# Performance work log

Hardware: AMD Instinct MI355X
Metric: run time of the kernel (lower is better)

## Reference

```python
import jax, jax.numpy as jnp
import numpy as np

N_NODES = 50000
N_EDGES = 800000
D_FEAT = 64


def setup_inputs() -> dict:
    key = jax.random.key(0)
    k1, k2, k3, k4 = jax.random.split(key, 4)
    row_idx = jnp.sort(jax.random.randint(k1, (N_EDGES,), 0, N_NODES, dtype=jnp.int32))
    col_idx = jax.random.randint(k2, (N_EDGES,), 0, N_NODES, dtype=jnp.int32)
    vals = jax.random.uniform(k3, (N_EDGES,), dtype=jnp.float32)
    embeds = jax.random.normal(k4, (N_NODES, D_FEAT), dtype=jnp.float32)
    return {"row_idx": row_idx, "col_idx": col_idx, "vals": vals, "embeds": embeds}


def reference(row_idx, col_idx, vals, embeds):
    # SpMM: out[r] = sum_{e: row[e]==r} vals[e] * embeds[col[e]]
    gathered = vals[:, None] * embeds[col_idx]          # [E, D]
    out = jax.ops.segment_sum(gathered, row_idx, num_segments=N_NODES)  # [N, D]
    return out
```

## Files before the change

kernel.cpp:

```cpp
#include <hip/hip_runtime.h>


constexpr int N_NODES = 50000;
constexpr int N_EDGES = 800000;
constexpr int D_FEAT  = 64;

__global__ __launch_bounds__(256) void build_row_ptr_kernel(
    const int* __restrict__ row_idx,
    int*       __restrict__ row_ptr)
{
    const int e = blockIdx.x * blockDim.x + threadIdx.x;
    if (e >= N_EDGES) return;
    const int r     = row_idx[e];
    const int rprev = (e == 0) ? -1 : row_idx[e - 1];
    for (int q = rprev + 1; q <= r; ++q) row_ptr[q] = e;
    if (e == N_EDGES - 1) {
        for (int q = r + 1; q <= N_NODES; ++q) row_ptr[q] = N_EDGES;
    }
}

__global__ __launch_bounds__(256) void gcn_spmm_rows_kernel(
    const int*   __restrict__ row_ptr,
    const int*   __restrict__ col_idx,
    const float* __restrict__ vals,
    const float* __restrict__ embeds,
    float*       __restrict__ out)
{
    const int gtid = blockIdx.x * blockDim.x + threadIdx.x;
    const int row  = gtid >> 6;
    const int lane = threadIdx.x & 63;
    if (row >= N_NODES) return;

    const int s = row_ptr[row];
    const int e = row_ptr[row + 1];

    float a0 = 0.f, a1 = 0.f, a2 = 0.f, a3 = 0.f;

    for (int base = s; base < e; base += 64) {
        const int n = (e - base < 64) ? (e - base) : 64;

        int   c = 0;
        float v = 0.f;
        if (lane < n) {
            c = col_idx[base + lane];
            v = vals[base + lane];
        }

        int j = 0;
        for (; j + 4 <= n; j += 4) {
            const int   c0 = __shfl(c, j);
            const int   c1 = __shfl(c, j + 1);
            const int   c2 = __shfl(c, j + 2);
            const int   c3 = __shfl(c, j + 3);
            const float v0 = __shfl(v, j);
            const float v1 = __shfl(v, j + 1);
            const float v2 = __shfl(v, j + 2);
            const float v3 = __shfl(v, j + 3);
            const float g0 = embeds[c0 * D_FEAT + lane];
            const float g1 = embeds[c1 * D_FEAT + lane];
            const float g2 = embeds[c2 * D_FEAT + lane];
            const float g3 = embeds[c3 * D_FEAT + lane];
            a0 += v0 * g0;
            a1 += v1 * g1;
            a2 += v2 * g2;
            a3 += v3 * g3;
        }
        for (; j < n; ++j) {
            const int   cj = __shfl(c, j);
            const float vj = __shfl(v, j);
            a0 += vj * embeds[cj * D_FEAT + lane];
        }
    }

    out[row * D_FEAT + lane] = (a0 + a1) + (a2 + a3);
}

extern "C" void kernel_launch(void* const* d_in, const int* in_sizes, int n_in,
                              void* d_out, int out_size, void* d_ws, size_t ws_size,
                              hipStream_t stream) {
    const int*   row_idx = (const int*)  d_in[0];
    const int*   col_idx = (const int*)  d_in[1];
    const float* vals    = (const float*)d_in[2];
    const float* embeds  = (const float*)d_in[3];
    float*       out     = (float*)      d_out;
    int*         row_ptr = (int*)        d_ws;

    {
        const int block  = 256;
        const int blocks = (N_EDGES + block - 1) / block;
        build_row_ptr_kernel<<<blocks, block, 0, stream>>>(row_idx, row_ptr);
    }

    {
        const int block  = 256;
        const int blocks = (N_NODES * 64 + block - 1) / block;
        gcn_spmm_rows_kernel<<<blocks, block, 0, stream>>>(row_ptr, col_idx, vals,
                                                           embeds, out);
    }
}
```

Before: 103.5 us.

## Split each row's edges across four sub-groups with float4 gathers and shuffle reduction

Each 64-lane wavefront now handles a row as four 16-lane groups. Each group reads a different edge directly and gathers the full 64-float embedding row as float4 loads, instead of broadcasting indices through shuffles and loading one float per lane. The partial sums are combined with xor shuffles, and one group writes a float4 result. This cuts the shuffle overhead and raises memory-level parallelism per row, in exchange for a reduction at the end and somewhat less coalesced loads of the edge indices.

```diff
diff --git a/kernel.cpp b/kernel.cpp
--- a/kernel.cpp
+++ b/kernel.cpp
@@ -28,51 +28,50 @@
 {
     const int gtid = blockIdx.x * blockDim.x + threadIdx.x;
     const int row  = gtid >> 6;
+    if (row >= N_NODES) return;
     const int lane = threadIdx.x & 63;
-    if (row >= N_NODES) return;
+    const int q    = lane >> 4;
+    const int f    = lane & 15;
 
     const int s = row_ptr[row];
     const int e = row_ptr[row + 1];
 
-    float a0 = 0.f, a1 = 0.f, a2 = 0.f, a3 = 0.f;
+    const float4* __restrict__ emb4 = (const float4*)embeds;
 
-    for (int base = s; base < e; base += 64) {
-        const int n = (e - base < 64) ? (e - base) : 64;
+    float4 a0 = make_float4(0.f, 0.f, 0.f, 0.f);
+    float4 a1 = make_float4(0.f, 0.f, 0.f, 0.f);
 
-        int   c = 0;
-        float v = 0.f;
-        if (lane < n) {
-            c = col_idx[base + lane];
-            v = vals[base + lane];
-        }
-
-        int j = 0;
-        for (; j + 4 <= n; j += 4) {
-            const int   c0 = __shfl(c, j);
-            const int   c1 = __shfl(c, j + 1);
-            const int   c2 = __shfl(c, j + 2);
-            const int   c3 = __shfl(c, j + 3);
-            const float v0 = __shfl(v, j);
-            const float v1 = __shfl(v, j + 1);
-            const float v2 = __shfl(v, j + 2);
-            const float v3 = __shfl(v, j + 3);
-            const float g0 = embeds[c0 * D_FEAT + lane];
-            const float g1 = embeds[c1 * D_FEAT + lane];
-            const float g2 = embeds[c2 * D_FEAT + lane];
-            const float g3 = embeds[c3 * D_FEAT + lane];
-            a0 += v0 * g0;
-            a1 += v1 * g1;
-            a2 += v2 * g2;
-            a3 += v3 * g3;
-        }
-        for (; j < n; ++j) {
-            const int   cj = __shfl(c, j);
-            const float vj = __shfl(v, j);
-            a0 += vj * embeds[cj * D_FEAT + lane];
-        }
+    int base = s + q;
+    for (; base + 4 < e; base += 8) {
+        const int   c0 = col_idx[base];
+        const float v0 = vals[base];
+        const int   c1 = col_idx[base + 4];
+        const float v1 = vals[base + 4];
+        const float4 g0 = emb4[c0 * 16 + f];
+        const float4 g1 = emb4[c1 * 16 + f];
+        a0.x += v0 * g0.x; a0.y += v0 * g0.y; a0.z += v0 * g0.z; a0.w += v0 * g0.w;
+        a1.x += v1 * g1.x; a1.y += v1 * g1.y; a1.z += v1 * g1.z; a1.w += v1 * g1.w;
+    }
+    if (base < e) {
+        const int   c0 = col_idx[base];
+        const float v0 = vals[base];
+        const float4 g0 = emb4[c0 * 16 + f];
+        a0.x += v0 * g0.x; a0.y += v0 * g0.y; a0.z += v0 * g0.z; a0.w += v0 * g0.w;
     }
 
-    out[row * D_FEAT + lane] = (a0 + a1) + (a2 + a3);
+    float x = a0.x + a1.x;
+    float y = a0.y + a1.y;
+    float z = a0.z + a1.z;
+    float w = a0.w + a1.w;
+
+    x += __shfl_xor(x, 16); x += __shfl_xor(x, 32);
+    y += __shfl_xor(y, 16); y += __shfl_xor(y, 32);
+    z += __shfl_xor(z, 16); z += __shfl_xor(z, 32);
+    w += __shfl_xor(w, 16); w += __shfl_xor(w, 32);
+
+    if (q == 0) {
+        ((float4*)out)[row * 16 + f] = make_float4(x, y, z, w);
+    }
 }
 
 extern "C" void kernel_launch(void* const* d_in, const int* in_sizes, int n_in,
@@ -90,7 +89,6 @@
         const int blocks = (N_EDGES + block - 1) / block;
         build_row_ptr_kernel<<<blocks, block, 0, stream>>>(row_idx, row_ptr);
     }
-
     {
         const int block  = 256;
         const int blocks = (N_NODES * 64 + block - 1) / block;
```

Measured after the change: 101.3 us. 2.1% less time.
